# Optimization experiments

Hardware: AMD Instinct MI355X
Metric: run time of the kernel (lower is better)

## Reference

```python
import jax, jax.numpy as jnp
import numpy as np

N = 50000
E = 600000
D_IN = 128
D_HID = 128


def gcn_conv(x, src, dst, ew, W, b):
    """PyG-style GCNConv with self-loops and symmetric normalization.
    x: [N, Fin], src/dst: [E'], ew: [E'], W: [Fin, Fout], b: [Fout].
    """
    n = x.shape[0]
    # degree from incoming edge weights (self-loops already appended)
    deg = jax.ops.segment_sum(ew, dst, num_segments=n)
    dinv = jnp.where(deg > 0, jax.lax.rsqrt(deg), 0.0)
    norm = dinv[src] * ew * dinv[dst]  # [E']
    h = x @ W  # linear transform first (PyG order)
    msg = h[src] * norm[:, None]  # gather + scale, [E', Fout]
    out = jax.ops.segment_sum(msg, dst, num_segments=n)  # scatter-add
    return out + b


def setup_inputs() -> dict:
    key = jax.random.key(0)
    k1, k2, k3, k4, k5, k6, k7 = jax.random.split(key, 7)
    x = jax.random.normal(k1, (N, D_IN), dtype=jnp.float32)
    edge_index = jax.random.randint(k2, (2, E), 0, N, dtype=jnp.int64)
    edge_weight = jax.random.uniform(k3, (E,), dtype=jnp.float32)
    s1 = 1.0 / np.sqrt(D_IN)
    s2 = 1.0 / np.sqrt(D_HID)
    W1 = jax.random.uniform(k4, (D_IN, D_HID), dtype=jnp.float32, minval=-s1, maxval=s1)
    b1 = jax.random.uniform(k5, (D_HID,), dtype=jnp.float32, minval=-s1, maxval=s1)
    W2 = jax.random.uniform(k6, (D_HID, D_IN), dtype=jnp.float32, minval=-s2, maxval=s2)
    b2 = jax.random.uniform(k7, (D_IN,), dtype=jnp.float32, minval=-s2, maxval=s2)
    return {"x": x, "edge_index": edge_index, "edge_weight": edge_weight,
            "W1": W1, "b1": b1, "W2": W2, "b2": b2}


def reference(x, edge_index, edge_weight, W1, b1, W2, b2):
    n = x.shape[0]
    loops = jnp.arange(n, dtype=edge_index.dtype)
    src = jnp.concatenate([edge_index[0], loops])
    dst = jnp.concatenate([edge_index[1], loops])
    ew = jnp.concatenate([edge_weight, jnp.ones((n,), dtype=edge_weight.dtype)])
    h = gcn_conv(x, src, dst, ew, W1, b1)
    h = jax.nn.relu(h)
    h = gcn_conv(h, src, dst, ew, W2, b2)
    return jax.nn.sigmoid(h)
```

## Files before the change

kernel.cpp:

```cpp
#include <hip/hip_runtime.h>
#include <math.h>


typedef unsigned int uint32;
typedef unsigned long long u64;
typedef __attribute__((ext_vector_type(8))) short bf16x8;
typedef __attribute__((ext_vector_type(4))) float f32x4;
typedef __attribute__((ext_vector_type(2))) float f32x2;

__device__ __forceinline__ unsigned short f2bf(float f) {
    uint32 b = __float_as_uint(f);
    return (unsigned short)((b + 0x7FFFu + ((b >> 16) & 1u)) >> 16);
}

__device__ __forceinline__ float2 bf2_decode(uint32 u) {
    return make_float2(__uint_as_float(u << 16),
                       __uint_as_float(u & 0xFFFF0000u));
}

template <int AFP32, int OUTFP8>
__device__ __forceinline__ void gemm_body(const void* __restrict__ Ap,
                                          const unsigned short* __restrict__ WT,
                                          void* __restrict__ H,
                                          int n, int tb) {
    const int lane = threadIdx.x & 63;
    const int wv   = threadIdx.x >> 6;
    const int quad = lane >> 4;
    const int l16  = lane & 15;
    const int m0   = tb * 128 + wv * 32;
    f32x4 acc[2][8] = {};

    #pragma unroll
    for (int ks = 0; ks < 4; ++ks) {
        const int k0 = ks * 32 + quad * 8;
        bf16x8 a[2];
        #pragma unroll
        for (int rt = 0; rt < 2; ++rt) {
            int row = m0 + rt * 16 + l16;
            if (row >= n) row = n - 1;
            if (AFP32) {
                const float* Af = (const float*)Ap + (size_t)row * 128 + k0;
                float4 f0 = *(const float4*)(Af);
                float4 f1 = *(const float4*)(Af + 4);
                bf16x8 v;
                v[0] = (short)f2bf(f0.x); v[1] = (short)f2bf(f0.y);
                v[2] = (short)f2bf(f0.z); v[3] = (short)f2bf(f0.w);
                v[4] = (short)f2bf(f1.x); v[5] = (short)f2bf(f1.y);
                v[6] = (short)f2bf(f1.z); v[7] = (short)f2bf(f1.w);
                a[rt] = v;
            } else {
                const unsigned short* Ab = (const unsigned short*)Ap + (size_t)row * 128 + k0;
                a[rt] = *(const bf16x8*)Ab;
            }
        }
        #pragma unroll
        for (int ct = 0; ct < 8; ++ct) {
            bf16x8 b = *(const bf16x8*)(WT + (size_t)(ct * 16 + l16) * 128 + k0);
            acc[0][ct] = __builtin_amdgcn_mfma_f32_16x16x32_bf16(a[0], b, acc[0][ct], 0, 0, 0);
            acc[1][ct] = __builtin_amdgcn_mfma_f32_16x16x32_bf16(a[1], b, acc[1][ct], 0, 0, 0);
        }
    }

    #pragma unroll
    for (int rt = 0; rt < 2; ++rt) {
        #pragma unroll
        for (int r = 0; r < 4; ++r) {
            int row = m0 + rt * 16 + quad * 4 + r;
            if (row < n) {
                if (OUTFP8) {
                    unsigned char* o = (unsigned char*)H + (size_t)row * 128 + l16;
                    #pragma unroll
                    for (int cp = 0; cp < 4; ++cp) {
                        int pk = __builtin_amdgcn_cvt_pk_fp8_f32(
                            acc[rt][2 * cp][r], acc[rt][2 * cp + 1][r], 0, false);
                        o[(2 * cp) * 16]     = (unsigned char)(pk & 0xFF);
                        o[(2 * cp + 1) * 16] = (unsigned char)((pk >> 8) & 0xFF);
                    }
                } else {
                    unsigned short* o = (unsigned short*)H + (size_t)row * 128 + l16;
                    #pragma unroll
                    for (int ct = 0; ct < 8; ++ct)
                        o[ct * 16] = f2bf(acc[rt][ct][r]);
                }
            }
        }
    }
}

__global__ __launch_bounds__(256) void k_init(u64* __restrict__ packed, int n4,
                                              int* __restrict__ done,
                                              const float* __restrict__ W1,
                                              const float* __restrict__ W2,
                                              unsigned short* __restrict__ WT1,
                                              unsigned short* __restrict__ WT2) {
    int idx = blockIdx.x * 256 + threadIdx.x;
    if (idx < n4) ((uint4*)packed)[idx] = make_uint4(0u, 0u, 0u, 0u);
    if (idx == 0) *done = 0;
    if (blockIdx.x < 64) {
        int j = blockIdx.x * 256 + threadIdx.x;
        int k = j >> 7, nn = j & 127;
        WT1[nn * 128 + k] = f2bf(W1[k * 128 + nn]);
        WT2[nn * 128 + k] = f2bf(W2[k * 128 + nn]);
    }
}

__global__ __launch_bounds__(256) void k_gemm1_hist(const float* __restrict__ x,
                                                    const unsigned short* __restrict__ WT1,
                                                    unsigned char* __restrict__ h8,
                                                    const int* __restrict__ dst,
                                                    const float* __restrict__ ew,
                                                    u64* __restrict__ packed,
                                                    int* __restrict__ rank,
                                                    int E, int N, int gGemm) {
    const int b = blockIdx.x;
    if (b < gGemm) {
        gemm_body<1, 1>(x, WT1, h8, N, b);
        return;
    }
    int i = (b - gGemm) * 256 + threadIdx.x;
    if (i < E) {
        int d = dst[i];
        int r = (i >> 8) & 7;
        u64 add = (1ULL << 44) + (u64)(ew[i] * 4294967296.0f);
        u64 old = atomicAdd(&packed[(size_t)r * N + d], add);
        rank[i] = (int)(old >> 44);
    }
}

__global__ __launch_bounds__(256) void k_scan(const u64* __restrict__ packed,
                                              float* __restrict__ dinv,
                                              u64* __restrict__ bases,
                                              int* __restrict__ rowptr,
                                              int* __restrict__ csums,
                                              int* __restrict__ done, int nNodes) {
    __shared__ int s[256];
    __shared__ int lastFlag;
    const int t = threadIdx.x;
    const int base = blockIdx.x * 1024 + t * 4;
    const int n = nNodes + 1;
    int v[4];
    #pragma unroll
    for (int u = 0; u < 4; ++u) {
        int idx = base + u;
        int c = 0;
        if (idx < nNodes) {
            const u64 mask = (1ULL << 44) - 1;
            u64 ssum = 0;
            u64 bs = 0;
            uint32 cum = 0;
            #pragma unroll
            for (int r = 0; r < 8; ++r) {
                u64 pv = packed[(size_t)r * nNodes + idx];
                bs |= (u64)cum << (8 * r);
                cum += (uint32)(pv >> 44);
                ssum += (pv & mask);
            }
            c = (int)cum;
            float deg = 1.0f + (float)ssum * (1.0f / 4294967296.0f);
            dinv[idx] = rsqrtf(deg);
            bases[idx] = bs;
        }
        v[u] = c;
    }
    s[t] = v[0] + v[1] + v[2] + v[3];
    __syncthreads();
    #pragma unroll
    for (int off = 1; off < 256; off <<= 1) {
        int x = (t >= off) ? s[t - off] : 0;
        __syncthreads();
        s[t] += x;
        __syncthreads();
    }
    if (t == 255)
        __hip_atomic_store(&csums[blockIdx.x], s[255], __ATOMIC_RELEASE,
                           __HIP_MEMORY_SCOPE_AGENT);
    int e = (t == 0) ? 0 : s[t - 1];
    if (base + 0 < n) rowptr[base + 0] = e;
    if (base + 1 < n) rowptr[base + 1] = e + v[0];
    if (base + 2 < n) rowptr[base + 2] = e + v[0] + v[1];
    if (base + 3 < n) rowptr[base + 3] = e + v[0] + v[1] + v[2];

    __syncthreads();
    if (t == 0) {
        int prev = __hip_atomic_fetch_add(done, 1, __ATOMIC_ACQ_REL,
                                          __HIP_MEMORY_SCOPE_AGENT);
        lastFlag = (prev == (int)gridDim.x - 1);
    }
    __syncthreads();
    if (lastFlag && t < 64) {
        int g = (int)gridDim.x;
        int orig = (t < g) ? __hip_atomic_load(&csums[t], __ATOMIC_ACQUIRE,
                                               __HIP_MEMORY_SCOPE_AGENT)
                           : 0;
        int vv = orig;
        #pragma unroll
        for (int off = 1; off < 64; off <<= 1) {
            int y = __shfl_up(vv, off, 64);
            if (t >= off) vv += y;
        }
        if (t < g) csums[t] = vv - orig;
    }
}

__global__ __launch_bounds__(256) void k_fill(const int* __restrict__ src,
                                              const int* __restrict__ dst,
                                              const float* __restrict__ ew,
                                              const float* __restrict__ dinv,
                                              const int* __restrict__ rowptr,
                                              const int* __restrict__ csums,
                                              const u64* __restrict__ bases,
                                              const int* __restrict__ rank,
                                              float2* __restrict__ csr, int e) {
    int i = blockIdx.x * 256 + threadIdx.x;
    if (i < e) {
        int s = src[i], d = dst[i];
        int r = (i >> 8) & 7;
        float nrm = dinv[s] * ew[i] * dinv[d];
        int pos = rowptr[d] + csums[d >> 10]
                + (int)((bases[d] >> (8 * r)) & 0xFF) + rank[i];
        csr[pos] = make_float2(__int_as_float(s), nrm);
    }
}

__global__ __launch_bounds__(256) void k_gemm2(const unsigned short* __restrict__ Ap,
                                               const unsigned short* __restrict__ WT,
                                               unsigned short* __restrict__ H, int n) {
    gemm_body<0, 0>(Ap, WT, H, n, blockIdx.x);
}

__device__ __forceinline__ void fma8_bf(float* acc, uint4 u, float w) {
    float2 f;
    f = bf2_decode(u.x); acc[0] += f.x * w; acc[1] += f.y * w;
    f = bf2_decode(u.y); acc[2] += f.x * w; acc[3] += f.y * w;
    f = bf2_decode(u.z); acc[4] += f.x * w; acc[5] += f.y * w;
    f = bf2_decode(u.w); acc[6] += f.x * w; acc[7] += f.y * w;
}

__device__ __forceinline__ void fma8_f8(float* acc, uint2 u, float w) {
    f32x2 f;
    f = __builtin_amdgcn_cvt_pk_f32_fp8((int)u.x, false);
    acc[0] += f[0] * w; acc[1] += f[1] * w;
    f = __builtin_amdgcn_cvt_pk_f32_fp8((int)u.x, true);
    acc[2] += f[0] * w; acc[3] += f[1] * w;
    f = __builtin_amdgcn_cvt_pk_f32_fp8((int)u.y, false);
    acc[4] += f[0] * w; acc[5] += f[1] * w;
    f = __builtin_amdgcn_cvt_pk_f32_fp8((int)u.y, true);
    acc[6] += f[0] * w; acc[7] += f[1] * w;
}

template <int INFP8, int ACT>
__global__ __launch_bounds__(256) void k_gather(const void* __restrict__ Hp,
                                                const float2* __restrict__ csr,
                                                const int* __restrict__ rowptr,
                                                const int* __restrict__ csums,
                                                const float* __restrict__ dinv,
                                                const float4* __restrict__ bias4,
                                                void* __restrict__ outp, int N) {
    int node = blockIdx.x * 4 + (threadIdx.x >> 6);
    if (node >= N) return;
    const int lane = threadIdx.x & 63;
    const int q = lane >> 4, l = lane & 15;
    const int start = rowptr[node] + csums[node >> 10];
    const int end   = rowptr[node + 1] + csums[(node + 1) >> 10];

    const uint2* H2 = (const uint2*)Hp;
    const uint4* H4 = (const uint4*)Hp;

    float di = dinv[node];
    float selfw = (q == 0) ? di * di : 0.0f;
    float acc[8] = {};
    if (INFP8) fma8_f8(acc, H2[(size_t)node * 16 + l], selfw);
    else       fma8_bf(acc, H4[(size_t)node * 16 + l], selfw);

    for (int k = start; k < end; k += 16) {
        float2 c[4];
        float w[4];
        #pragma unroll
        for (int j = 0; j < 4; ++j) {
            int ej = k + q + 4 * j;
            c[j] = csr[ej < end ? ej : end - 1];
            w[j] = (ej < end) ? c[j].y : 0.0f;
        }
        if (INFP8) {
            uint2 u[4];
            #pragma unroll
            for (int j = 0; j < 4; ++j)
                u[j] = H2[(size_t)__float_as_int(c[j].x) * 16 + l];
            #pragma unroll
            for (int j = 0; j < 4; ++j) fma8_f8(acc, u[j], w[j]);
        } else {
            uint4 u[4];
            #pragma unroll
            for (int j = 0; j < 4; ++j)
                u[j] = H4[(size_t)__float_as_int(c[j].x) * 16 + l];
            #pragma unroll
            for (int j = 0; j < 4; ++j) fma8_bf(acc, u[j], w[j]);
        }
    }

    #pragma unroll
    for (int j = 0; j < 8; ++j) {
        acc[j] += __shfl_xor(acc[j], 16, 64);
        acc[j] += __shfl_xor(acc[j], 32, 64);
    }

    if (q == 0) {
        float4 b0 = bias4[l * 2], b1 = bias4[l * 2 + 1];
        acc[0] += b0.x; acc[1] += b0.y; acc[2] += b0.z; acc[3] += b0.w;
        acc[4] += b1.x; acc[5] += b1.y; acc[6] += b1.z; acc[7] += b1.w;
        if (ACT == 0) {
            #pragma unroll
            for (int j = 0; j < 8; ++j) acc[j] = fmaxf(acc[j], 0.0f);
            uint4 o;
            o.x = (uint32)f2bf(acc[0]) | ((uint32)f2bf(acc[1]) << 16);
            o.y = (uint32)f2bf(acc[2]) | ((uint32)f2bf(acc[3]) << 16);
            o.z = (uint32)f2bf(acc[4]) | ((uint32)f2bf(acc[5]) << 16);
            o.w = (uint32)f2bf(acc[6]) | ((uint32)f2bf(acc[7]) << 16);
            ((uint4*)outp)[(size_t)node * 16 + l] = o;
        } else {
            #pragma unroll
            for (int j = 0; j < 8; ++j) acc[j] = 1.0f / (1.0f + expf(-acc[j]));
            float4* o4 = (float4*)outp + (size_t)node * 32 + l * 2;
            o4[0] = make_float4(acc[0], acc[1], acc[2], acc[3]);
            o4[1] = make_float4(acc[4], acc[5], acc[6], acc[7]);
        }
    }
}

extern "C" void kernel_launch(void* const* d_in, const int* in_sizes, int n_in,
                              void* d_out, int out_size, void* d_ws, size_t ws_size,
                              hipStream_t stream) {
    const float* x  = (const float*)d_in[0];
    const int*   ei = (const int*)d_in[1];
    const float* ew = (const float*)d_in[2];
    const float* W1 = (const float*)d_in[3];
    const float* b1 = (const float*)d_in[4];
    const float* W2 = (const float*)d_in[5];
    const float* b2 = (const float*)d_in[6];

    const int N = in_sizes[0] / 128;
    const int E = in_sizes[2];
    const int* src = ei;
    const int* dst = ei + E;
    float* out = (float*)d_out;

    auto align = [](size_t v) { return (v + 255) & ~(size_t)255; };
    char* p = (char*)d_ws;
    float*  dinv   = (float*)p;   p += align((size_t)N * 4);
    int*    rowptr = (int*)p;     p += align((size_t)(N + 1) * 4);
    int*    csums  = (int*)p;     p += align((size_t)1024 * 4);
    int*    done   = (int*)p;     p += align((size_t)256);
    u64*    bases  = (u64*)p;     p += align((size_t)N * 8);
    unsigned short* WT1 = (unsigned short*)p; p += align((size_t)128 * 128 * 2);
    unsigned short* WT2 = (unsigned short*)p; p += align((size_t)128 * 128 * 2);
    int*    rank   = (int*)p;     p += align((size_t)E * 4);
    float2* csr    = (float2*)p;  p += align((size_t)E * 8);
    unsigned char*  h8 = (unsigned char*)p;  p += align((size_t)N * 128);
    unsigned short* h2 = (unsigned short*)p; p += align((size_t)N * 128 * 2);
    unsigned short* g1 = (unsigned short*)p;
    u64* packed = (u64*)g1;

    const int nbE = (E + 255) / 256;
    const int gScan = (N + 1 + 1023) / 1024;
    const int gGemm = (N + 127) / 128;
    const int gGath = (N + 3) / 4;
    const int n4 = N * 4;
    const int gInit = ((n4 + 255) / 256) < 64 ? 64 : ((n4 + 255) / 256);

    k_init<<<gInit, 256, 0, stream>>>(packed, n4, done, W1, W2, WT1, WT2);
    k_gemm1_hist<<<gGemm + nbE, 256, 0, stream>>>(x, WT1, h8, dst, ew, packed,
                                                  rank, E, N, gGemm);
    k_scan<<<gScan, 256, 0, stream>>>(packed, dinv, bases, rowptr, csums, done, N);
    k_fill<<<nbE, 256, 0, stream>>>(src, dst, ew, dinv, rowptr, csums, bases,
                                    rank, csr, E);

    k_gather<1, 0><<<gGath, 256, 0, stream>>>(h8, csr, rowptr, csums,
                                              dinv, (const float4*)b1, g1, N);

    k_gemm2<<<gGemm, 256, 0, stream>>>(g1, WT2, h2, N);
    k_gather<0, 1><<<gGath, 256, 0, stream>>>(h2, csr, rowptr, csums,
                                              dinv, (const float4*)b2, out, N);
}
```

Baseline: 210.2 us.

## Fuse layer-1 aggregation with layer-2 GEMM through shared memory

```diff
diff --git a/kernel.cpp b/kernel.cpp
--- a/kernel.cpp
+++ b/kernel.cpp
@@ -222,12 +222,6 @@
     }
 }
 
-__global__ __launch_bounds__(256) void k_gemm2(const unsigned short* __restrict__ Ap,
-                                               const unsigned short* __restrict__ WT,
-                                               unsigned short* __restrict__ H, int n) {
-    gemm_body<0, 0>(Ap, WT, H, n, blockIdx.x);
-}
-
 __device__ __forceinline__ void fma8_bf(float* acc, uint4 u, float w) {
     float2 f;
     f = bf2_decode(u.x); acc[0] += f.x * w; acc[1] += f.y * w;
@@ -246,6 +240,102 @@
     acc[4] += f[0] * w; acc[5] += f[1] * w;
     f = __builtin_amdgcn_cvt_pk_f32_fp8((int)u.y, true);
     acc[6] += f[0] * w; acc[7] += f[1] * w;
+}
+
+__global__ __launch_bounds__(256) void k_ag2(const unsigned char* __restrict__ h8,
+                                             const float2* __restrict__ csr,
+                                             const int* __restrict__ rowptr,
+                                             const int* __restrict__ csums,
+                                             const float* __restrict__ dinv,
+                                             const float4* __restrict__ bias4,
+                                             const unsigned short* __restrict__ WT2,
+                                             unsigned short* __restrict__ h2,
+                                             int N) {
+    __shared__ unsigned short sA[32][136];
+    const int lane = threadIdx.x & 63;
+    const int wv   = threadIdx.x >> 6;
+    const int q    = lane >> 4;
+    const int l    = lane & 15;
+    const int nb   = blockIdx.x * 32;
+    const uint2* H2 = (const uint2*)h8;
+
+    for (int j = 0; j < 8; ++j) {
+        const int node = nb + wv * 8 + j;
+        float acc[8] = {};
+        if (node < N) {
+            const int start = rowptr[node] + csums[node >> 10];
+            const int end   = rowptr[node + 1] + csums[(node + 1) >> 10];
+            float di = dinv[node];
+            float selfw = (q == 0) ? di * di : 0.0f;
+            fma8_f8(acc, H2[(size_t)node * 16 + l], selfw);
+
+            for (int k = start; k < end; k += 16) {
+                float2 c[4];
+                float w[4];
+                #pragma unroll
+                for (int jj = 0; jj < 4; ++jj) {
+                    int ej = k + q + 4 * jj;
+                    c[jj] = csr[ej < end ? ej : end - 1];
+                    w[jj] = (ej < end) ? c[jj].y : 0.0f;
+                }
+                uint2 u[4];
+                #pragma unroll
+                for (int jj = 0; jj < 4; ++jj)
+                    u[jj] = H2[(size_t)__float_as_int(c[jj].x) * 16 + l];
+                #pragma unroll
+                for (int jj = 0; jj < 4; ++jj) fma8_f8(acc, u[jj], w[jj]);
+            }
+            #pragma unroll
+            for (int t = 0; t < 8; ++t) {
+                acc[t] += __shfl_xor(acc[t], 16, 64);
+                acc[t] += __shfl_xor(acc[t], 32, 64);
+            }
+        }
+        if (q == 0) {
+            uint4 o = make_uint4(0u, 0u, 0u, 0u);
+            if (node < N) {
+                float4 b0 = bias4[l * 2], b1v = bias4[l * 2 + 1];
+                acc[0] += b0.x;  acc[1] += b0.y;  acc[2] += b0.z;  acc[3] += b0.w;
+                acc[4] += b1v.x; acc[5] += b1v.y; acc[6] += b1v.z; acc[7] += b1v.w;
+                #pragma unroll
+                for (int t = 0; t < 8; ++t) acc[t] = fmaxf(acc[t], 0.0f);
+                o.x = (uint32)f2bf(acc[0]) | ((uint32)f2bf(acc[1]) << 16);
+                o.y = (uint32)f2bf(acc[2]) | ((uint32)f2bf(acc[3]) << 16);
+                o.z = (uint32)f2bf(acc[4]) | ((uint32)f2bf(acc[5]) << 16);
+                o.w = (uint32)f2bf(acc[6]) | ((uint32)f2bf(acc[7]) << 16);
+            }
+            *(uint4*)&sA[wv * 8 + j][l * 8] = o;
+        }
+    }
+
+    __syncthreads();
+
+    f32x4 a2[2][2] = {};
+    #pragma unroll
+    for (int ks = 0; ks < 4; ++ks) {
+        const int k0 = ks * 32 + q * 8;
+        bf16x8 a[2];
+        a[0] = *(const bf16x8*)&sA[l][k0];
+        a[1] = *(const bf16x8*)&sA[16 + l][k0];
+        #pragma unroll
+        for (int ct = 0; ct < 2; ++ct) {
+            bf16x8 b = *(const bf16x8*)(WT2 + (size_t)(wv * 32 + ct * 16 + l) * 128 + k0);
+            a2[0][ct] = __builtin_amdgcn_mfma_f32_16x16x32_bf16(a[0], b, a2[0][ct], 0, 0, 0);
+            a2[1][ct] = __builtin_amdgcn_mfma_f32_16x16x32_bf16(a[1], b, a2[1][ct], 0, 0, 0);
+        }
+    }
+    #pragma unroll
+    for (int rt = 0; rt < 2; ++rt) {
+        #pragma unroll
+        for (int r = 0; r < 4; ++r) {
+            int row = nb + rt * 16 + q * 4 + r;
+            if (row < N) {
+                unsigned short* o = h2 + (size_t)row * 128 + wv * 32 + l;
+                o[0]  = f2bf(a2[rt][0][r]);
+                o[16] = f2bf(a2[rt][1][r]);
+            }
+        }
+    }
 }
 
 template <int INFP8, int ACT>
@@ -356,14 +446,14 @@
     int*    rank   = (int*)p;     p += align((size_t)E * 4);
     float2* csr    = (float2*)p;  p += align((size_t)E * 8);
     unsigned char*  h8 = (unsigned char*)p;  p += align((size_t)N * 128);
-    unsigned short* h2 = (unsigned short*)p; p += align((size_t)N * 128 * 2);
-    unsigned short* g1 = (unsigned short*)p;
-    u64* packed = (u64*)g1;
+    unsigned short* h2 = (unsigned short*)p;
+    u64* packed = (u64*)h2;
 
     const int nbE = (E + 255) / 256;
     const int gScan = (N + 1 + 1023) / 1024;
     const int gGemm = (N + 127) / 128;
     const int gGath = (N + 3) / 4;
+    const int gAg2  = (N + 31) / 32;
     const int n4 = N * 4;
     const int gInit = ((n4 + 255) / 256) < 64 ? 64 : ((n4 + 255) / 256);
 
@@ -374,10 +464,9 @@
     k_fill<<<nbE, 256, 0, stream>>>(src, dst, ew, dinv, rowptr, csums, bases,
                                     rank, csr, E);
 
-    k_gather<1, 0><<<gGath, 256, 0, stream>>>(h8, csr, rowptr, csums,
-                                              dinv, (const float4*)b1, g1, N);
-
-    k_gemm2<<<gGemm, 256, 0, stream>>>(g1, WT2, h2, N);
+    k_ag2<<<gAg2, 256, 0, stream>>>(h8, csr, rowptr, csums, dinv,
+                                    (const float4*)b1, WT2, h2, N);
+
     k_gather<0, 1><<<gGath, 256, 0, stream>>>(h2, csr, rowptr, csums,
                                               dinv, (const float4*)b2, out, N);
 }
```

After: 214.3 us. No clear change (+1.9%).
